# Optimization experiments

Measured on AMD Instinct MI355X. Metric: run time of the kernel, lower is better.

## Reference

```python
import jax, jax.numpy as jnp
import numpy as np

IMG_SIZE = 32
PATCH_SIZE = 4
GRID = IMG_SIZE // PATCH_SIZE  # 8 -> 64 patches
EMBED = 768
PATCH_DIM = 1 * 3 * PATCH_SIZE * PATCH_SIZE  # 48
BATCH = 1024


def setup_inputs() -> dict:
    key = jax.random.key(0)
    k1, k2, k3, k4 = jax.random.split(key, 4)
    x = jax.random.normal(k1, (BATCH, 1, 3, IMG_SIZE, IMG_SIZE), dtype=jnp.float32)
    W = jax.random.normal(k2, (EMBED, PATCH_DIM), dtype=jnp.float32) * 0.02  # fc1.weight [out,in]
    cls_token = jax.random.normal(k3, (1, EMBED), dtype=jnp.float32)
    pos_emb = jax.random.normal(k4, (1, GRID * GRID + 1, EMBED), dtype=jnp.float32)
    return {"x": x, "W": W, "cls_token": cls_token, "pos_emb": pos_emb}


def reference(x, W, cls_token, pos_emb):
    B, D1, C, H, Wd = x.shape
    # Row-major patch extraction matching the loop (col fast, row slow).
    # patch flatten order = (D1, C, ph, pw), identical to nn.Flatten(1) on [B,D1,C,P,P].
    patches = x.reshape(B, D1, C, GRID, PATCH_SIZE, GRID, PATCH_SIZE)
    patches = patches.transpose(0, 3, 5, 1, 2, 4, 6)  # [B, gr, gc, D1, C, P, P]
    patches = patches.reshape(B, GRID * GRID, D1 * C * PATCH_SIZE * PATCH_SIZE)  # [B,64,48]
    proj = jnp.einsum('bnp,ep->bne', patches, W)  # fc1 (no bias) -> [B,64,E]
    cls = jnp.broadcast_to(cls_token[None, :, :], (B, 1, EMBED))
    s = jnp.concatenate([cls, proj], axis=1)  # [B,65,E]
    return pos_emb + s
```

## Files before the change

### kernel.cpp

```cpp
#include <hip/hip_runtime.h>


#define BATCH   1024
#define EMBED   768
#define NPATCH  64
#define SEQ     65
#define OUTB    (SEQ * EMBED)
#define WELEMS  (EMBED * 48)

typedef __attribute__((ext_vector_type(8))) short bf16x8;
typedef __attribute__((ext_vector_type(4))) float f32x4;

__device__ __forceinline__ short f2bf(float f) {
    union { float f; unsigned u; } v; v.f = f;
    unsigned r = v.u + 0x7FFFu + ((v.u >> 16) & 1u);
    return (short)(r >> 16);
}

__global__ __launch_bounds__(256) void prep_kernel(const float* __restrict__ W,
                                                   const float* __restrict__ cls,
                                                   const float* __restrict__ pos,
                                                   short* __restrict__ w16,
                                                   float* __restrict__ out) {
    const int tid = threadIdx.x;
    const int bid = blockIdx.x;
    if (bid < 18) {
        const int i = (bid * 256 + tid) * 8;
        float4 u0 = *(const float4*)(W + i);
        float4 u1 = *(const float4*)(W + i + 4);
        bf16x8 v;
        v[0] = f2bf(u0.x); v[1] = f2bf(u0.y); v[2] = f2bf(u0.z); v[3] = f2bf(u0.w);
        v[4] = f2bf(u1.x); v[5] = f2bf(u1.y); v[6] = f2bf(u1.z); v[7] = f2bf(u1.w);
        *(bf16x8*)(w16 + i) = v;
    } else {
        const int b = bid - 18;
        if (tid < 192) {
            f32x4 cv = ((const f32x4*)cls)[tid];
            f32x4 pv = ((const f32x4*)pos)[tid];
            ((f32x4*)out)[(size_t)b * (OUTB / 4) + tid] = cv + pv;
        }
    }
}

__global__ __launch_bounds__(256, 4) void patch_embed_main(const float* __restrict__ x,
                                                           const short* __restrict__ w16,
                                                           const float* __restrict__ pos,
                                                           float* __restrict__ out) {
    __shared__ short A[64 * 64];

    const int tid  = threadIdx.x;
    const int lane = tid & 63;
    const int wave = tid >> 6;
    const int lr   = lane & 15;
    const int lg   = lane >> 4;
    const int bid  = blockIdx.x;
    const int b    = bid >> 1;
    const int eh   = bid & 1;
    const int ebase = eh * 384 + wave * 96;

    #pragma unroll
    for (int i = 0; i < 2; ++i) {
        const int cid = tid + i * 256;
        const int row = cid >> 3;
        const int kb  = cid & 7;
        short* dst = &A[row * 64 + ((kb ^ (row & 7)) * 8)];
        bf16x8 v = {0, 0, 0, 0, 0, 0, 0, 0};
        if (kb < 6) {
            const int c   = kb >> 1;
            const int ph0 = (kb & 1) * 2;
            const int gr = row >> 3, gc = row & 7;
            const float* src = x + (size_t)b * 3072 + c * 1024 + (gr * 4 + ph0) * 32 + gc * 4;
            float4 u0 = *(const float4*)src;
            float4 u1 = *(const float4*)(src + 32);
            v[0] = f2bf(u0.x); v[1] = f2bf(u0.y); v[2] = f2bf(u0.z); v[3] = f2bf(u0.w);
            v[4] = f2bf(u1.x); v[5] = f2bf(u1.y); v[6] = f2bf(u1.z); v[7] = f2bf(u1.w);
        }
        *(bf16x8*)dst = v;
    }

    bf16x8 bw[6][2];
    #pragma unroll
    for (int nt = 0; nt < 6; ++nt) {
        const short* wrow = w16 + (ebase + nt * 16 + lr) * 48;
        bw[nt][0] = *(const bf16x8*)(wrow + lg * 8);
        const int k1 = 32 + lg * 8;
        bf16x8 f = {0, 0, 0, 0, 0, 0, 0, 0};
        if (k1 < 48) f = *(const bf16x8*)(wrow + k1);
        bw[nt][1] = f;
    }

    __syncthreads();

    const size_t outb = (size_t)b * OUTB + EMBED;
    const f32x4 zero = {0.f, 0.f, 0.f, 0.f};
    #pragma unroll 1
    for (int mt = 0; mt < 4; ++mt) {
        float pv[4][6];
        #pragma unroll
        for (int j = 0; j < 4; ++j) {
            const int n = mt * 16 + lg * 4 + j;
            const float* pr = pos + (size_t)(n + 1) * EMBED + ebase + lr;
            #pragma unroll
            for (int nt = 0; nt < 6; ++nt) pv[j][nt] = pr[nt * 16];
        }

        const int arow = mt * 16 + lr;
        bf16x8 a0 = *(const bf16x8*)&A[arow * 64 + ((lg ^ (arow & 7)) * 8)];
        bf16x8 a1 = *(const bf16x8*)&A[arow * 64 + (((4 + lg) ^ (arow & 7)) * 8)];

        f32x4 acc[6];
        #pragma unroll
        for (int nt = 0; nt < 6; ++nt)
            acc[nt] = __builtin_amdgcn_mfma_f32_16x16x32_bf16(a0, bw[nt][0], zero, 0, 0, 0);
        #pragma unroll
        for (int nt = 0; nt < 6; ++nt)
            acc[nt] = __builtin_amdgcn_mfma_f32_16x16x32_bf16(a1, bw[nt][1], acc[nt], 0, 0, 0);

        #pragma unroll
        for (int j = 0; j < 4; ++j) {
            const int n = mt * 16 + lg * 4 + j;
            float* orow = out + outb + (size_t)n * EMBED + ebase + lr;
            #pragma unroll
            for (int nt = 0; nt < 6; ++nt)
                orow[nt * 16] = acc[nt][j] + pv[j][nt];
        }
    }
}

extern "C" void kernel_launch(void* const* d_in, const int* in_sizes, int n_in,
                              void* d_out, int out_size, void* d_ws, size_t ws_size,
                              hipStream_t stream) {
    const float* x   = (const float*)d_in[0];
    const float* W   = (const float*)d_in[1];
    const float* cls = (const float*)d_in[2];
    const float* pos = (const float*)d_in[3];
    float* out = (float*)d_out;
    short* w16 = (short*)d_ws;

    hipLaunchKernelGGL(prep_kernel, dim3(18 + BATCH), dim3(256), 0, stream,
                       W, cls, pos, w16, out);
    hipLaunchKernelGGL(patch_embed_main, dim3(BATCH * 2), dim3(256), 0, stream,
                       x, w16, pos, out);
}
```

Before: 46.22 us.

## Pre-pack bf16 patch fragments in prep kernel, drop LDS staging from main kernel

Moves patch extraction and bf16 conversion into the prep kernel, which writes each batch's A operand to workspace already laid out in MFMA fragment order. The main kernel then loads A fragments directly from global memory with no shared memory and no barrier, and its occupancy hint is removed. This avoids the main kernel's duplicated per-half x reads and its LDS round trip. In exchange it adds an extra global write and read of about 8 MB of packed patches, plus more prep blocks.

```diff
diff --git a/kernel.cpp b/kernel.cpp
--- a/kernel.cpp
+++ b/kernel.cpp
@@ -3,10 +3,10 @@
 
 #define BATCH   1024
 #define EMBED   768
-#define NPATCH  64
 #define SEQ     65
 #define OUTB    (SEQ * EMBED)
-#define WELEMS  (EMBED * 48)
+#define WSPAT   (BATCH * 4096)
+#define W16OFF  WSPAT
 
 typedef __attribute__((ext_vector_type(8))) short bf16x8;
 typedef __attribute__((ext_vector_type(4))) float f32x4;
@@ -17,23 +17,48 @@
     return (short)(r >> 16);
 }
 
-__global__ __launch_bounds__(256) void prep_kernel(const float* __restrict__ W,
+__global__ __launch_bounds__(256) void prep_kernel(const float* __restrict__ x,
+                                                   const float* __restrict__ W,
                                                    const float* __restrict__ cls,
                                                    const float* __restrict__ pos,
-                                                   short* __restrict__ w16,
+                                                   short* __restrict__ ws,
                                                    float* __restrict__ out) {
     const int tid = threadIdx.x;
     const int bid = blockIdx.x;
-    if (bid < 18) {
-        const int i = (bid * 256 + tid) * 8;
+    if (bid < BATCH) {
+        const int b = bid;
+        #pragma unroll
+        for (int i = 0; i < 2; ++i) {
+            const int cid = tid + i * 256;
+            const int mt  = cid >> 7;
+            const int kk  = (cid >> 6) & 1;
+            const int lr  = cid & 15;
+            const int lg  = (cid >> 4) & 3;
+            const int kb  = kk * 4 + lg;
+            bf16x8 v = {0, 0, 0, 0, 0, 0, 0, 0};
+            if (kb < 6) {
+                const int row = mt * 16 + lr;
+                const int c   = kb >> 1;
+                const int ph0 = (kb & 1) * 2;
+                const int gr = row >> 3, gc = row & 7;
+                const float* src = x + (size_t)b * 3072 + c * 1024 + (gr * 4 + ph0) * 32 + gc * 4;
+                float4 u0 = *(const float4*)src;
+                float4 u1 = *(const float4*)(src + 32);
+                v[0] = f2bf(u0.x); v[1] = f2bf(u0.y); v[2] = f2bf(u0.z); v[3] = f2bf(u0.w);
+                v[4] = f2bf(u1.x); v[5] = f2bf(u1.y); v[6] = f2bf(u1.z); v[7] = f2bf(u1.w);
+            }
+            *(bf16x8*)(ws + ((size_t)b * 512 + cid) * 8) = v;
+        }
+    } else if (bid < BATCH + 18) {
+        const int i = ((bid - BATCH) * 256 + tid) * 8;
         float4 u0 = *(const float4*)(W + i);
         float4 u1 = *(const float4*)(W + i + 4);
         bf16x8 v;
         v[0] = f2bf(u0.x); v[1] = f2bf(u0.y); v[2] = f2bf(u0.z); v[3] = f2bf(u0.w);
         v[4] = f2bf(u1.x); v[5] = f2bf(u1.y); v[6] = f2bf(u1.z); v[7] = f2bf(u1.w);
-        *(bf16x8*)(w16 + i) = v;
+        *(bf16x8*)(ws + W16OFF + i) = v;
     } else {
-        const int b = bid - 18;
+        const int b = bid - (BATCH + 18);
         if (tid < 192) {
             f32x4 cv = ((const f32x4*)cls)[tid];
             f32x4 pv = ((const f32x4*)pos)[tid];
@@ -42,12 +67,9 @@
     }
 }
 
-__global__ __launch_bounds__(256, 4) void patch_embed_main(const float* __restrict__ x,
-                                                           const short* __restrict__ w16,
-                                                           const float* __restrict__ pos,
-                                                           float* __restrict__ out) {
-    __shared__ short A[64 * 64];
-
+__global__ __launch_bounds__(256) void patch_embed_main(const short* __restrict__ ws,
+                                                        const float* __restrict__ pos,
+                                                        float* __restrict__ out) {
     const int tid  = threadIdx.x;
     const int lane = tid & 63;
     const int wave = tid >> 6;
@@ -58,26 +80,7 @@
     const int eh   = bid & 1;
     const int ebase = eh * 384 + wave * 96;
 
-    #pragma unroll
-    for (int i = 0; i < 2; ++i) {
-        const int cid = tid + i * 256;
-        const int row = cid >> 3;
-        const int kb  = cid & 7;
-        short* dst = &A[row * 64 + ((kb ^ (row & 7)) * 8)];
-        bf16x8 v = {0, 0, 0, 0, 0, 0, 0, 0};
-        if (kb < 6) {
-            const int c   = kb >> 1;
-            const int ph0 = (kb & 1) * 2;
-            const int gr = row >> 3, gc = row & 7;
-            const float* src = x + (size_t)b * 3072 + c * 1024 + (gr * 4 + ph0) * 32 + gc * 4;
-            float4 u0 = *(const float4*)src;
-            float4 u1 = *(const float4*)(src + 32);
-            v[0] = f2bf(u0.x); v[1] = f2bf(u0.y); v[2] = f2bf(u0.z); v[3] = f2bf(u0.w);
-            v[4] = f2bf(u1.x); v[5] = f2bf(u1.y); v[6] = f2bf(u1.z); v[7] = f2bf(u1.w);
-        }
-        *(bf16x8*)dst = v;
-    }
-
+    const short* w16 = ws + W16OFF;
     bf16x8 bw[6][2];
     #pragma unroll
     for (int nt = 0; nt < 6; ++nt) {
@@ -89,24 +92,22 @@
         bw[nt][1] = f;
     }
 
-    __syncthreads();
-
+    const short* wsb = ws + (size_t)b * 4096;
     const size_t outb = (size_t)b * OUTB + EMBED;
     const f32x4 zero = {0.f, 0.f, 0.f, 0.f};
+
     #pragma unroll 1
     for (int mt = 0; mt < 4; ++mt) {
+        bf16x8 a0 = *(const bf16x8*)(wsb + ((mt * 2 + 0) * 64 + lane) * 8);
+        bf16x8 a1 = *(const bf16x8*)(wsb + ((mt * 2 + 1) * 64 + lane) * 8);
+
         float pv[4][6];
         #pragma unroll
         for (int j = 0; j < 4; ++j) {
-            const int n = mt * 16 + lg * 4 + j;
-            const float* pr = pos + (size_t)(n + 1) * EMBED + ebase + lr;
+            const float* pr = pos + (size_t)(mt * 16 + lg * 4 + j + 1) * EMBED + ebase + lr;
             #pragma unroll
             for (int nt = 0; nt < 6; ++nt) pv[j][nt] = pr[nt * 16];
         }
-
-        const int arow = mt * 16 + lr;
-        bf16x8 a0 = *(const bf16x8*)&A[arow * 64 + ((lg ^ (arow & 7)) * 8)];
-        bf16x8 a1 = *(const bf16x8*)&A[arow * 64 + (((4 + lg) ^ (arow & 7)) * 8)];
 
         f32x4 acc[6];
         #pragma unroll
@@ -135,10 +136,10 @@
     const float* cls = (const float*)d_in[2];
     const float* pos = (const float*)d_in[3];
     float* out = (float*)d_out;
-    short* w16 = (short*)d_ws;
+    short* ws  = (short*)d_ws;
 
-    hipLaunchKernelGGL(prep_kernel, dim3(18 + BATCH), dim3(256), 0, stream,
-                       W, cls, pos, w16, out);
+    hipLaunchKernelGGL(prep_kernel, dim3(BATCH + 18 + BATCH), dim3(256), 0, stream,
+                       x, W, cls, pos, ws, out);
     hipLaunchKernelGGL(patch_embed_main, dim3(BATCH * 2), dim3(256), 0, stream,
-                       x, w16, pos, out);
+                       ws, pos, out);
 }
```

Result: no change. 45.85 us (-0.8%).
